# Kernel tuning notes

Hardware: AMD Instinct MI355X
Metric: run time of the kernel (lower is better)

## Reference

```python
import jax, jax.numpy as jnp
import numpy as np

K = 4          # neighbor_num
BN_EPS = 1e-5


def setup_inputs() -> dict:
    key = jax.random.key(0)
    ks = jax.random.split(key, 5)
    b, n, c = 16384, 12, 512
    x = jax.random.normal(ks[0], (b, n, c), dtype=jnp.float32)
    std = np.sqrt(2.0 / c).astype(np.float32)
    Uw = jax.random.normal(ks[1], (c, c), dtype=jnp.float32) * std
    Vw = jax.random.normal(ks[2], (c, c), dtype=jnp.float32) * std
    bound = 1.0 / np.sqrt(c)
    Ub = jax.random.uniform(ks[3], (c,), minval=-bound, maxval=bound, dtype=jnp.float32)
    Vb = jax.random.uniform(ks[4], (c,), minval=-bound, maxval=bound, dtype=jnp.float32)
    gamma = jnp.ones((n,), dtype=jnp.float32)
    beta = jnp.zeros((n,), dtype=jnp.float32)
    return {"x": x, "Uw": Uw, "Ub": Ub, "Vw": Vw, "Vb": Vb, "gamma": gamma, "beta": beta}


def reference(x, Uw, Ub, Vw, Vb, gamma, beta):
    # x: [b, n, c] with n = num_classes nodes
    # ---- dynamic top-k adjacency ('dots' metric), built on detached x ----
    si = jax.lax.stop_gradient(x)
    sim = jnp.einsum('bic,bjc->bij', si, si)                 # [b, n, n]
    thr = jax.lax.top_k(sim, K)[0][..., -1:]                 # k-th largest per row
    adj = (sim >= thr).astype(x.dtype)                       # [b, n, n]
    # ---- normalize_digraph: D^{-1/2} A D^{-1/2} (row degrees) ----
    deg_inv_sqrt = adj.sum(axis=-1) ** -0.5                  # [b, n]
    A = deg_inv_sqrt[:, :, None] * adj * deg_inv_sqrt[:, None, :]
    # ---- aggregate + projections ----
    Vx = jnp.einsum('bnc,dc->bnd', x, Vw) + Vb               # V(x)
    agg = jnp.einsum('bij,bjc->bic', A, Vx)
    h = agg + jnp.einsum('bnc,dc->bnd', x, Uw) + Ub          # aggregate + U(x)
    # ---- BatchNorm1d over node channel n (stats over batch and feature dims) ----
    mean = h.mean(axis=(0, 2))                               # [n]
    var = ((h - mean[None, :, None]) ** 2).mean(axis=(0, 2)) # biased var, [n]
    hn = (h - mean[None, :, None]) * jax.lax.rsqrt(var + BN_EPS)[None, :, None]
    hn = hn * gamma[None, :, None] + beta[None, :, None]
    return jax.nn.relu(x + hn)
```

## Files before the change

kernel.cpp:

```cpp
#include <hip/hip_runtime.h>
#include <hip/hip_fp16.h>


typedef _Float16 half8 __attribute__((ext_vector_type(8)));
typedef _Float16 half4 __attribute__((ext_vector_type(4)));
typedef float floatx4 __attribute__((ext_vector_type(4)));

#define NN 12
#define CH 512
#define NB 16384
#define M_ROWS (NB * NN)

__device__ __forceinline__ float relu_f(float v) { return v > 0.f ? v : 0.f; }

__device__ __forceinline__ void gload16(const void* g, void* l) {
    __builtin_amdgcn_global_load_lds(
        (__attribute__((address_space(1))) const unsigned int*)g,
        (__attribute__((address_space(3))) unsigned int*)l, 16, 0, 0);
}

__global__ __launch_bounds__(256) void kw_build(const float* __restrict__ Uw,
                                                const float* __restrict__ Vw,
                                                _Float16* __restrict__ Wcat,
                                                double* __restrict__ gAcc) {
    int e = blockIdx.x * 256 + threadIdx.x;
    int d = e >> 10, k = e & 1023;
    float v = (k < 512) ? Uw[d * 512 + k] : Vw[d * 512 + (k - 512)];
    Wcat[e] = (_Float16)v;
    if (blockIdx.x == 0 && threadIdx.x < 24) gAcc[threadIdx.x] = 0.0;
}

__global__ __launch_bounds__(256) void k1_adj(const float* __restrict__ x,
                                              _Float16* __restrict__ Abuf,
                                              float* __restrict__ rs,
                                              int pathA) {
    __shared__ float xs[NN][CH + 4];
    __shared__ double psum[78][3];
    __shared__ double sim[NN][NN];
    __shared__ double thr[NN];
    __shared__ float Amat[NN][NN];
    __shared__ float dinv[NN];

    const int b = blockIdx.x, t = threadIdx.x;
    const float* xb = x + (size_t)b * NN * CH;

    for (int e = t; e < NN * CH / 4; e += 256) {
        int r = e >> 7, c4 = (e & 127) << 2;
        float4 v = ((const float4*)xb)[e];
        *(float4*)&xs[r][c4] = v;
    }
    __syncthreads();

    if (t < 234) {
        const int p = t / 3, s = t - p * 3;
        int i = 0, rem = p;
        while (rem >= NN - i) { rem -= NN - i; i++; }
        const int j = i + rem;
        const int c0 = (s == 0) ? 0 : (s == 1 ? 176 : 352);
        const int c1 = (s == 0) ? 176 : (s == 1 ? 352 : 512);
        double a0 = 0.0, a1 = 0.0, a2 = 0.0, a3 = 0.0;
        for (int c = c0; c < c1; c += 4) {
            float4 va = *(const float4*)&xs[i][c];
            float4 vb = *(const float4*)&xs[j][c];
            a0 += (double)va.x * (double)vb.x;
            a1 += (double)va.y * (double)vb.y;
            a2 += (double)va.z * (double)vb.z;
            a3 += (double)va.w * (double)vb.w;
        }
        psum[p][s] = (a0 + a1) + (a2 + a3);
    }
    __syncthreads();

    if (t < 78) {
        int i = 0, rem = t;
        while (rem >= NN - i) { rem -= NN - i; i++; }
        const int j = i + rem;
        double acc = (psum[t][0] + psum[t][1]) + psum[t][2];
        sim[i][j] = acc;
        sim[j][i] = acc;
    }
    __syncthreads();

    if (t < 12) {
        double a = -1e300, b2 = -1e300, c2 = -1e300, d2 = -1e300;
        for (int j = 0; j < 12; j++) {
            double v = sim[t][j];
            if (v > a)       { d2 = c2; c2 = b2; b2 = a; a = v; }
            else if (v > b2) { d2 = c2; c2 = b2; b2 = v; }
            else if (v > c2) { d2 = c2; c2 = v; }
            else if (v > d2) { d2 = v; }
        }
        thr[t] = d2;
        int deg = 0;
        for (int j = 0; j < 12; j++) deg += (sim[t][j] >= d2);
        dinv[t] = 1.0f / sqrtf((float)deg);
    }
    __syncthreads();

    if (t < 144) {
        int i = t / 12, j = t % 12;
        Amat[i][j] = (sim[i][j] >= thr[i]) ? dinv[i] * dinv[j] : 0.0f;
    }
    __syncthreads();

    if (t < 12) {
        float s = 0.f;
        for (int j = 0; j < 12; j++) s += Amat[t][j];
        rs[b * NN + t] = s;
    }

    const size_t strideK = pathA ? 1024 : 512;
    const size_t yoff = pathA ? 512 : 0;
    for (int e = t; e < NN * CH / 4; e += 256) {
        int i = e >> 7, c4 = (e & 127) << 2;
        float ax = 0.f, ay = 0.f, az = 0.f, aw = 0.f;
#pragma unroll
        for (int j = 0; j < 12; j++) {
            const float a = Amat[i][j];
            float4 v = *(const float4*)&xs[j][c4];
            ax += a * v.x; ay += a * v.y; az += a * v.z; aw += a * v.w;
        }
        const size_t row = (size_t)b * NN + i;
        half4 hy;
        hy[0] = (_Float16)ax; hy[1] = (_Float16)ay;
        hy[2] = (_Float16)az; hy[3] = (_Float16)aw;
        *(half4*)(Abuf + row * strideK + yoff + c4) = hy;
        if (pathA) {
            float4 xv = *(const float4*)&xs[i][c4];
            half4 hx;
            hx[0] = (_Float16)xv.x; hx[1] = (_Float16)xv.y;
            hx[2] = (_Float16)xv.z; hx[3] = (_Float16)xv.w;
            *(half4*)(Abuf + row * 1024 + c4) = hx;
        }
    }
}

__global__ __launch_bounds__(256) void k2_gemm(
    const _Float16* __restrict__ Abuf, const float* __restrict__ xf,
    const _Float16* __restrict__ Wcat, const float* __restrict__ rs,
    const float* __restrict__ Ub, const float* __restrict__ Vb,
    float* __restrict__ hout, _Float16* __restrict__ hout16,
    double* __restrict__ gS1, double* __restrict__ gS2, int pathA, int hpath) {
    __shared__ __align__(16) _Float16 As[2][128 * 32];
    __shared__ __align__(16) _Float16 Bs[2][128 * 32];
    __shared__ float bs1[12], bs2[12];

    const int t = threadIdx.x;
    const int bid = blockIdx.x;
    const int xcd = bid & 7, jj = bid >> 3;
    const int nt = jj & 3, mt = (jj >> 2) * 8 + xcd;
    const int m0 = mt * 128, n0 = nt * 128;
    const int lane = t & 63, wv = t >> 6;
    const int l15 = lane & 15, quad = lane >> 4;
    const int mwb = (wv & 1) * 64, nwb = (wv >> 1) * 64;
    const int srow = t >> 2, qs = t & 3;
    const int fsw = (srow >> 1) & 3;
    const int scol = (qs ^ fsw) * 8;

    floatx4 acc[4][4];
#pragma unroll
    for (int mi = 0; mi < 4; mi++)
#pragma unroll
        for (int ni = 0; ni < 4; ni++)
#pragma unroll
            for (int e = 0; e < 4; e++) acc[mi][ni][e] = 0.f;

    auto stage = [&](int buf, int kt) {
        const int k0 = kt * 32;
#pragma unroll
        for (int pass = 0; pass < 2; pass++) {
            const int row = srow + pass * 64;
            const size_t grow = (size_t)(m0 + row);
            _Float16* la = &As[buf][pass * 2048 + wv * 512];
            _Float16* lb = &Bs[buf][pass * 2048 + wv * 512];
            if (pathA) {
                gload16(Abuf + grow * 1024 + k0 + scol, la);
            } else if (k0 < 512) {
                const float* p = xf + grow * 512 + k0 + scol;
                float4 f0 = *(const float4*)p;
                float4 f1 = *(const float4*)(p + 4);
                half8 va;
                va[0] = (_Float16)f0.x; va[1] = (_Float16)f0.y;
                va[2] = (_Float16)f0.z; va[3] = (_Float16)f0.w;
                va[4] = (_Float16)f1.x; va[5] = (_Float16)f1.y;
                va[6] = (_Float16)f1.z; va[7] = (_Float16)f1.w;
                *(half8*)&As[buf][row * 32 + qs * 8] = va;
            } else {
                gload16(Abuf + grow * 512 + (k0 - 512) + scol, la);
            }
            gload16(Wcat + (size_t)(n0 + row) * 1024 + k0 + scol, lb);
        }
    };

    stage(0, 0);
    __syncthreads();

    const int rcol = (quad ^ ((l15 >> 1) & 3)) * 8;

    int cur = 0;
    for (int kt = 0; kt < 32; kt++) {
        if (kt < 31) stage(cur ^ 1, kt + 1);

        half8 af[4], bfr[4];
#pragma unroll
        for (int mi = 0; mi < 4; mi++)
            af[mi] = *(half8*)&As[cur][(mwb + mi * 16 + l15) * 32 + rcol];
#pragma unroll
        for (int ni = 0; ni < 4; ni++)
            bfr[ni] = *(half8*)&Bs[cur][(nwb + ni * 16 + l15) * 32 + rcol];
#pragma unroll
        for (int mi = 0; mi < 4; mi++)
#pragma unroll
            for (int ni = 0; ni < 4; ni++)
                acc[mi][ni] = __builtin_amdgcn_mfma_f32_16x16x32_f16(
                    af[mi], bfr[ni], acc[mi][ni], 0, 0, 0);

        __syncthreads();
        cur ^= 1;
    }

    if (t < 12) { bs1[t] = 0.f; bs2[t] = 0.f; }
    __syncthreads();
#pragma unroll
    for (int mi = 0; mi < 4; mi++) {
#pragma unroll
        for (int r = 0; r < 4; r++) {
            const int m = m0 + mwb + mi * 16 + quad * 4 + r;
            const float rsm = rs[m];
            float p1 = 0.f, p2 = 0.f;
#pragma unroll
            for (int ni = 0; ni < 4; ni++) {
                const int d = n0 + nwb + ni * 16 + l15;
                float h = acc[mi][ni][r] + rsm * Vb[d] + Ub[d];
                if (hpath) hout16[(size_t)m * 512 + d] = (_Float16)h;
                else       hout[(size_t)m * 512 + d] = h;
                p1 += h; p2 += h * h;
            }
            for (int off = 1; off < 16; off <<= 1) {
                p1 += __shfl_xor(p1, off, 16);
                p2 += __shfl_xor(p2, off, 16);
            }
            if (l15 == 0) {
                atomicAdd(&bs1[m % 12], p1);
                atomicAdd(&bs2[m % 12], p2);
            }
        }
    }
    __syncthreads();
    if (t < 12) {
        atomicAdd(&gS1[t], (double)bs1[t]);
        atomicAdd(&gS2[t], (double)bs2[t]);
    }
}

__global__ void k3_stats(const double* __restrict__ gS1,
                         const double* __restrict__ gS2,
                         const float* __restrict__ gamma,
                         const float* __restrict__ beta,
                         float* __restrict__ bnp) {
    int t = threadIdx.x;
    if (t < 12) {
        const double cnt = (double)NB * 512.0;
        double mean = gS1[t] / cnt;
        double var = gS2[t] / cnt - mean * mean;
        float inv = rsqrtf((float)var + 1e-5f);
        float scale = gamma[t] * inv;
        bnp[t] = scale;
        bnp[12 + t] = beta[t] - (float)mean * scale;
    }
}

__global__ __launch_bounds__(256) void k4_final(const float* __restrict__ x,
                                                float* __restrict__ out,
                                                const _Float16* __restrict__ h16,
                                                const float* __restrict__ bnp,
                                                int hpath) {
    __shared__ float sc[12], sh[12];
    if (threadIdx.x < 12) {
        sc[threadIdx.x] = bnp[threadIdx.x];
        sh[threadIdx.x] = bnp[12 + threadIdx.x];
    }
    __syncthreads();
    const size_t n4 = (size_t)M_ROWS * 128;
    for (size_t i = (size_t)blockIdx.x * 256 + threadIdx.x; i < n4;
         i += (size_t)gridDim.x * 256) {
        int m = (int)(i >> 7);
        int n = m % 12;
        float4 h;
        if (hpath) {
            half4 hv = *(const half4*)(h16 + i * 4);
            h.x = (float)hv[0]; h.y = (float)hv[1];
            h.z = (float)hv[2]; h.w = (float)hv[3];
        } else {
            h = ((const float4*)out)[i];
        }
        float4 xv = ((const float4*)x)[i];
        float s = sc[n], b = sh[n];
        float4 r;
        r.x = relu_f(xv.x + h.x * s + b);
        r.y = relu_f(xv.y + h.y * s + b);
        r.z = relu_f(xv.z + h.z * s + b);
        r.w = relu_f(xv.w + h.w * s + b);
        ((float4*)out)[i] = r;
    }
}

extern "C" void kernel_launch(void* const* d_in, const int* in_sizes, int n_in,
                              void* d_out, int out_size, void* d_ws,
                              size_t ws_size, hipStream_t stream) {
    const float* x     = (const float*)d_in[0];
    const float* Uw    = (const float*)d_in[1];
    const float* Ub    = (const float*)d_in[2];
    const float* Vw    = (const float*)d_in[3];
    const float* Vb    = (const float*)d_in[4];
    const float* gamma = (const float*)d_in[5];
    const float* beta  = (const float*)d_in[6];
    float* out = (float*)d_out;

    const size_t szA  = (size_t)M_ROWS * 1024 * 2;
    const size_t szB  = (size_t)M_ROWS * 512 * 2;
    const size_t szW  = (size_t)512 * 1024 * 2;
    const size_t szrs = (size_t)M_ROWS * 4;
    const size_t szH  = (size_t)M_ROWS * 512 * 2;
    const size_t needA = szA + szW + szrs + 24 * 8 + 24 * 4;
    const int pathA = (ws_size >= needA) ? 1 : 0;
    const int hpath = (pathA && ws_size >= needA + szH) ? 1 : 0;

    char* w = (char*)d_ws;
    _Float16* Abuf = (_Float16*)w;
    const size_t big = pathA ? szA : szB;
    _Float16* Wcat = (_Float16*)(w + big);
    float* rs      = (float*)(w + big + szW);
    double* gS1    = (double*)(w + big + szW + szrs);
    double* gS2    = gS1 + 12;
    float* bnp     = (float*)(gS2 + 12);
    _Float16* Hbuf = (_Float16*)(w + needA);

    kw_build<<<2048, 256, 0, stream>>>(Uw, Vw, Wcat, gS1);
    k1_adj<<<NB, 256, 0, stream>>>(x, Abuf, rs, pathA);
    k2_gemm<<<(M_ROWS / 128) * 4, 256, 0, stream>>>(Abuf, x, Wcat, rs, Ub, Vb,
                                                    out, Hbuf, gS1, gS2, pathA,
                                                    hpath);
    k3_stats<<<1, 64, 0, stream>>>(gS1, gS2, gamma, beta, bnp);
    k4_final<<<4096, 256, 0, stream>>>(x, out, Hbuf, bnp, hpath);
}
```

Measured before the change: 1.235 ms.

## Triple-buffer GEMM pipeline with explicit waitcnt and register-cached adjacency aggregation

```diff
diff --git a/kernel.cpp b/kernel.cpp
--- a/kernel.cpp
+++ b/kernel.cpp
@@ -38,7 +38,7 @@
     __shared__ double psum[78][3];
     __shared__ double sim[NN][NN];
     __shared__ double thr[NN];
-    __shared__ float Amat[NN][NN];
+    __shared__ __align__(16) float Amat[NN][NN];
     __shared__ float dinv[NN];
 
     const int b = blockIdx.x, t = threadIdx.x;
@@ -109,28 +109,39 @@
         rs[b * NN + t] = s;
     }
 
+    const int c4e = (t & 127) << 2;
+    const int ih0 = (t >> 7) * 6;
+    float4 xv[12];
+#pragma unroll
+    for (int j = 0; j < 12; j++) xv[j] = *(const float4*)&xs[j][c4e];
+
     const size_t strideK = pathA ? 1024 : 512;
     const size_t yoff = pathA ? 512 : 0;
-    for (int e = t; e < NN * CH / 4; e += 256) {
-        int i = e >> 7, c4 = (e & 127) << 2;
+#pragma unroll
+    for (int ii = 0; ii < 6; ii++) {
+        const int i = ih0 + ii;
+        const float4 a0 = *(const float4*)&Amat[i][0];
+        const float4 a1 = *(const float4*)&Amat[i][4];
+        const float4 a2 = *(const float4*)&Amat[i][8];
+        const float ar[12] = {a0.x, a0.y, a0.z, a0.w, a1.x, a1.y,
+                              a1.z, a1.w, a2.x, a2.y, a2.z, a2.w};
         float ax = 0.f, ay = 0.f, az = 0.f, aw = 0.f;
 #pragma unroll
         for (int j = 0; j < 12; j++) {
-            const float a = Amat[i][j];
-            float4 v = *(const float4*)&xs[j][c4];
-            ax += a * v.x; ay += a * v.y; az += a * v.z; aw += a * v.w;
+            ax += ar[j] * xv[j].x; ay += ar[j] * xv[j].y;
+            az += ar[j] * xv[j].z; aw += ar[j] * xv[j].w;
         }
         const size_t row = (size_t)b * NN + i;
         half4 hy;
         hy[0] = (_Float16)ax; hy[1] = (_Float16)ay;
         hy[2] = (_Float16)az; hy[3] = (_Float16)aw;
-        *(half4*)(Abuf + row * strideK + yoff + c4) = hy;
+        *(half4*)(Abuf + row * strideK + yoff + c4e) = hy;
         if (pathA) {
-            float4 xv = *(const float4*)&xs[i][c4];
+            const float4 xr = xv[i];
             half4 hx;
-            hx[0] = (_Float16)xv.x; hx[1] = (_Float16)xv.y;
-            hx[2] = (_Float16)xv.z; hx[3] = (_Float16)xv.w;
-            *(half4*)(Abuf + row * 1024 + c4) = hx;
+            hx[0] = (_Float16)xr.x; hx[1] = (_Float16)xr.y;
+            hx[2] = (_Float16)xr.z; hx[3] = (_Float16)xr.w;
+            *(half4*)(Abuf + row * 1024 + c4e) = hx;
         }
     }
 }
@@ -141,8 +152,8 @@
     const float* __restrict__ Ub, const float* __restrict__ Vb,
     float* __restrict__ hout, _Float16* __restrict__ hout16,
     double* __restrict__ gS1, double* __restrict__ gS2, int pathA, int hpath) {
-    __shared__ __align__(16) _Float16 As[2][128 * 32];
-    __shared__ __align__(16) _Float16 Bs[2][128 * 32];
+    __shared__ __align__(16) _Float16 As[3][128 * 32];
+    __shared__ __align__(16) _Float16 Bs[3][128 * 32];
     __shared__ float bs1[12], bs2[12];
 
     const int t = threadIdx.x;
@@ -156,6 +167,7 @@
     const int srow = t >> 2, qs = t & 3;
     const int fsw = (srow >> 1) & 3;
     const int scol = (qs ^ fsw) * 8;
+    const int rcol = (quad ^ ((l15 >> 1) & 3)) * 8;
 
     floatx4 acc[4][4];
 #pragma unroll
@@ -170,53 +182,92 @@
 #pragma unroll
         for (int pass = 0; pass < 2; pass++) {
             const int row = srow + pass * 64;
-            const size_t grow = (size_t)(m0 + row);
-            _Float16* la = &As[buf][pass * 2048 + wv * 512];
-            _Float16* lb = &Bs[buf][pass * 2048 + wv * 512];
-            if (pathA) {
-                gload16(Abuf + grow * 1024 + k0 + scol, la);
-            } else if (k0 < 512) {
-                const float* p = xf + grow * 512 + k0 + scol;
-                float4 f0 = *(const float4*)p;
-                float4 f1 = *(const float4*)(p + 4);
-                half8 va;
-                va[0] = (_Float16)f0.x; va[1] = (_Float16)f0.y;
-                va[2] = (_Float16)f0.z; va[3] = (_Float16)f0.w;
-                va[4] = (_Float16)f1.x; va[5] = (_Float16)f1.y;
-                va[6] = (_Float16)f1.z; va[7] = (_Float16)f1.w;
-                *(half8*)&As[buf][row * 32 + qs * 8] = va;
-            } else {
-                gload16(Abuf + grow * 512 + (k0 - 512) + scol, la);
-            }
-            gload16(Wcat + (size_t)(n0 + row) * 1024 + k0 + scol, lb);
+            gload16(Abuf + (size_t)(m0 + row) * 1024 + k0 + scol,
+                    &As[buf][pass * 2048 + wv * 512]);
+            gload16(Wcat + (size_t)(n0 + row) * 1024 + k0 + scol,
+                    &Bs[buf][pass * 2048 + wv * 512]);
         }
     };
 
-    stage(0, 0);
-    __syncthreads();
-
-    const int rcol = (quad ^ ((l15 >> 1) & 3)) * 8;
-
-    int cur = 0;
-    for (int kt = 0; kt < 32; kt++) {
-        if (kt < 31) stage(cur ^ 1, kt + 1);
-
+    auto compute = [&](int cb) {
         half8 af[4], bfr[4];
 #pragma unroll
         for (int mi = 0; mi < 4; mi++)
-            af[mi] = *(half8*)&As[cur][(mwb + mi * 16 + l15) * 32 + rcol];
+            af[mi] = *(half8*)&As[cb][(mwb + mi * 16 + l15) * 32 + rcol];
 #pragma unroll
         for (int ni = 0; ni < 4; ni++)
-            bfr[ni] = *(half8*)&Bs[cur][(nwb + ni * 16 + l15) * 32 + rcol];
+            bfr[ni] = *(half8*)&Bs[cb][(nwb + ni * 16 + l15) * 32 + rcol];
+        __builtin_amdgcn_s_setprio(1);
 #pragma unroll
         for (int mi = 0; mi < 4; mi++)
 #pragma unroll
             for (int ni = 0; ni < 4; ni++)
                 acc[mi][ni] = __builtin_amdgcn_mfma_f32_16x16x32_f16(
                     af[mi], bfr[ni], acc[mi][ni], 0, 0, 0);
-
+        __builtin_amdgcn_s_setprio(0);
+    };
+
+    if (pathA) {
+        stage(0, 0); stage(1, 1); stage(2, 2);
+        int cur = 0;
+#pragma unroll 1
+        for (int kt = 0; kt < 29; kt++) {
+            asm volatile("s_waitcnt vmcnt(8)" ::: "memory");
+            __builtin_amdgcn_s_barrier();
+            __builtin_amdgcn_sched_barrier(0);
+            compute(cur);
+            asm volatile("s_waitcnt lgkmcnt(0)" ::: "memory");
+            __builtin_amdgcn_s_barrier();
+            __builtin_amdgcn_sched_barrier(0);
+            stage(cur, kt + 3);
+            cur = (cur == 2) ? 0 : cur + 1;
+        }
+        asm volatile("s_waitcnt vmcnt(8)" ::: "memory");
+        __builtin_amdgcn_s_barrier();
+        __builtin_amdgcn_sched_barrier(0);
+        compute(2);
+        asm volatile("s_waitcnt vmcnt(4)" ::: "memory");
+        __builtin_amdgcn_s_barrier();
+        __builtin_amdgcn_sched_barrier(0);
+        compute(0);
+        asm volatile("s_waitcnt vmcnt(0)" ::: "memory");
+        __builtin_amdgcn_s_barrier();
+        __builtin_amdgcn_sched_barrier(0);
+        compute(1);
+    } else {
+        auto stageB = [&](int buf, int kt) {
+            const int k0 = kt * 32;
+#pragma unroll
+            for (int pass = 0; pass < 2; pass++) {
+                const int row = srow + pass * 64;
+                const size_t grow = (size_t)(m0 + row);
+                if (k0 < 512) {
+                    const float* p = xf + grow * 512 + k0 + scol;
+                    float4 f0 = *(const float4*)p;
+                    float4 f1 = *(const float4*)(p + 4);
+                    half8 va;
+                    va[0] = (_Float16)f0.x; va[1] = (_Float16)f0.y;
+                    va[2] = (_Float16)f0.z; va[3] = (_Float16)f0.w;
+                    va[4] = (_Float16)f1.x; va[5] = (_Float16)f1.y;
+                    va[6] = (_Float16)f1.z; va[7] = (_Float16)f1.w;
+                    *(half8*)&As[buf][row * 32 + qs * 8] = va;
+                } else {
+                    gload16(Abuf + grow * 512 + (k0 - 512) + scol,
+                            &As[buf][pass * 2048 + wv * 512]);
+                }
+                gload16(Wcat + (size_t)(n0 + row) * 1024 + k0 + scol,
+                        &Bs[buf][pass * 2048 + wv * 512]);
+            }
+        };
+        stageB(0, 0);
         __syncthreads();
-        cur ^= 1;
+        int cur = 0;
+        for (int kt = 0; kt < 32; kt++) {
+            if (kt < 31) stageB(cur ^ 1, kt + 1);
+            compute(cur);
+            __syncthreads();
+            cur ^= 1;
+        }
     }
 
     if (t < 12) { bs1[t] = 0.f; bs2[t] = 0.f; }
```

New measurement: 1.647 ms. +33.3%, slower.
